# Optimization experiments

Measured on AMD Instinct MI355X. Metric: run time of the kernel, lower is better.

The kernel has to match this reference:

```python
import jax, jax.numpy as jnp
import numpy as np

NUM_LAYERS = 2


def setup_inputs() -> dict:
    key = jax.random.key(0)
    k1, k2, k3, k4 = jax.random.split(key, 4)
    N, E, D = 50000, 800000, 100
    features = jax.random.normal(k1, (N, D), dtype=jnp.float32)
    # stacked nn.Linear weights, one [D,D] per layer (no bias)
    W = jax.random.normal(k2, (NUM_LAYERS, D, D), dtype=jnp.float32) * 0.02
    src = jax.random.randint(k3, (E,), 0, N)
    dst = jax.random.randint(k4, (E,), 0, N)
    return {"features": features, "W": W, "src": src, "dst": dst}


def reference(features, W, src, dst):
    N, D = features.shape
    num_layers = W.shape[0]
    inv_lp1 = 1.0 / (num_layers + 1)

    # --- graph preprocessing (mirrors ItemConv.graph setter) ---
    # add self loops (fill_diag 1.0), then row-normalize by inverse degree
    loop = jnp.arange(N)
    src_all = jnp.concatenate([src, loop])  # message sources
    dst_all = jnp.concatenate([dst, loop])  # message destinations (rows of adj_t)
    deg = jax.ops.segment_sum(
        jnp.ones(src_all.shape, dtype=features.dtype), dst_all, num_segments=N
    )
    deg_inv = jnp.where(deg > 0, 1.0 / deg, 0.0)
    w = deg_inv[dst_all]  # per-edge weight: row-normalized, [E+N]

    # --- forward (LightGCN-style conv with linear projections) ---
    avg = features * inv_lp1
    x = features
    for i in range(num_layers):
        x = x @ W[i].T  # nn.Linear(D, D, bias=False)
        # SpMM: out[d] = sum_{e: dst=d} w_e * x[src_e]
        x = jax.ops.segment_sum(w[:, None] * x[src_all], dst_all, num_segments=N)
        # F.normalize(x): L2 along dim=-1 with eps=1e-12 (max-clamped norm)
        norm = jnp.linalg.norm(x, axis=-1, keepdims=True)
        avg = avg + (x / jnp.maximum(norm, 1e-12)) * inv_lp1
    return avg
```

## Files before the change

kernel.cpp:

```cpp
#include <hip/hip_runtime.h>

#define D 100
#define YSTRIDE 128
#define BSHIFT 7
#define BSIZE 128
#define BMASK 127
#define NBKMAX 512
#define EPB 2048
#define BCAP 4096
#define WTOT (2 * 7 * 4 * 64)

typedef __attribute__((ext_vector_type(8))) short bf8v;
typedef __attribute__((ext_vector_type(4))) float f4v;

__device__ inline unsigned short f2bf(float f) {
    unsigned u = __float_as_uint(f);
    return (unsigned short)((u + 0x7fffu + ((u >> 16) & 1u)) >> 16);
}
__device__ inline float bflo(unsigned v) { return __uint_as_float(v << 16); }
__device__ inline float bfhi(unsigned v) { return __uint_as_float(v & 0xffff0000u); }
__device__ inline unsigned short pk8(float a, float b) {
    return (unsigned short)(__builtin_amdgcn_cvt_pk_fp8_f32(a, b, 0, false) & 0xffff);
}

__device__ inline void acc8(float* acc, uint2 v, float w) {
    acc[0] = fmaf(__builtin_amdgcn_cvt_f32_fp8((int)v.x, 0), w, acc[0]);
    acc[1] = fmaf(__builtin_amdgcn_cvt_f32_fp8((int)v.x, 1), w, acc[1]);
    acc[2] = fmaf(__builtin_amdgcn_cvt_f32_fp8((int)v.x, 2), w, acc[2]);
    acc[3] = fmaf(__builtin_amdgcn_cvt_f32_fp8((int)v.x, 3), w, acc[3]);
    acc[4] = fmaf(__builtin_amdgcn_cvt_f32_fp8((int)v.y, 0), w, acc[4]);
    acc[5] = fmaf(__builtin_amdgcn_cvt_f32_fp8((int)v.y, 1), w, acc[5]);
    acc[6] = fmaf(__builtin_amdgcn_cvt_f32_fp8((int)v.y, 2), w, acc[6]);
    acc[7] = fmaf(__builtin_amdgcn_cvt_f32_fp8((int)v.y, 3), w, acc[7]);
}

__device__ inline void scan512_excl(int* a, int* t, int tid) {
    int v0 = a[2 * tid], v1 = a[2 * tid + 1];
    t[tid] = v0 + v1;
    __syncthreads();
    for (int off = 1; off < 256; off <<= 1) {
        int u = (tid >= off) ? t[tid - off] : 0;
        __syncthreads();
        t[tid] += u;
        __syncthreads();
    }
    int base = (tid ? t[tid - 1] : 0);
    a[2 * tid]     = base;
    a[2 * tid + 1] = base + v0;
    __syncthreads();
}

__global__ __launch_bounds__(256) void k_pre(const float* __restrict__ x0, const float* __restrict__ W,
                                             unsigned* __restrict__ s8, float* __restrict__ Wc,
                                             int* __restrict__ cur,
                                             int N, int packb) {
    int tid = threadIdx.x;
    int bx = blockIdx.x;

    if (bx < packb) {
        int t = bx * 256 + tid;
        if (t >= N * 32) return;
        int d = t >> 5, q = t & 31;
        unsigned p = 0u;
        if (q < D / 4) {
            float4 v = *(const float4*)(x0 + (long)d * D + q * 4);
            p = (unsigned)pk8(v.x, v.y) | ((unsigned)pk8(v.z, v.w) << 16);
        }
        s8[t] = p;
    } else if (bx == packb) {
        cur[tid] = 0;
        cur[tid + 256] = 0;
    } else {
        int t = (bx - packb - 1) * 256 + tid;
        if (t >= D * D) return;
        int i = t / D, j = t - i * D;
        const float* w2 = W + D * D + (long)i * D;
        float s = 0.f;
        for (int k = 0; k < D; k++) s += w2[k] * W[(long)k * D + j];
        Wc[t] = s;
    }
}

__global__ __launch_bounds__(256) void k_sortC(const int* __restrict__ src,
                                               const int* __restrict__ dst,
                                               int* __restrict__ cur,
                                               unsigned* __restrict__ ebuf, int E, int nbk,
                                               int nebk,
                                               const float* __restrict__ W1,
                                               const float* __restrict__ Wc,
                                               unsigned short* __restrict__ P) {
    __shared__ int lhist[NBKMAX], lstart[NBKMAX], runS[NBKMAX], t[256];
    __shared__ unsigned stage[EPB];
    int tid = threadIdx.x;

    if ((int)blockIdx.x >= nebk) {
        int t2 = ((int)blockIdx.x - nebk) * 256 + tid;
        if (t2 >= WTOT) return;
        int lane = t2 & 63;
        int r = t2 >> 6;
        int kt = r & 3;
        int r2 = r >> 2;
        int nt = r2 % 7;
        int l  = r2 / 7;
        const float* M = (l == 0) ? W1 : Wc;
        int ng = nt * 16 + (lane & 15);
        int k0 = kt * 32 + (lane >> 4) * 8;
        unsigned short u[8];
#pragma unroll
        for (int j = 0; j < 8; j++) {
            int k = k0 + j;
            u[j] = (ng < D && k < D) ? f2bf(M[(long)ng * D + k]) : (unsigned short)0;
        }
        uint4 o;
        o.x = (unsigned)u[0] | ((unsigned)u[1] << 16);
        o.y = (unsigned)u[2] | ((unsigned)u[3] << 16);
        o.z = (unsigned)u[4] | ((unsigned)u[5] << 16);
        o.w = (unsigned)u[6] | ((unsigned)u[7] << 16);
        *(uint4*)(P + (long)t2 * 8) = o;
        return;
    }

    int base = blockIdx.x * EPB;
    int count = min(EPB, E - base);

    for (int i = tid; i < NBKMAX; i += 256) lhist[i] = 0;
    __syncthreads();
    for (int i = tid; i < count; i += 256) atomicAdd(&lhist[dst[base + i] >> BSHIFT], 1);
    __syncthreads();
    for (int i = tid; i < NBKMAX; i += 256) lstart[i] = lhist[i];
    __syncthreads();
    scan512_excl(lstart, t, tid);
    for (int b = tid; b < nbk; b += 256) {
        int c = lhist[b];
        runS[b] = b * BCAP + (c ? atomicAdd(&cur[b], c) : 0);
    }
    __syncthreads();
    for (int i = tid; i < NBKMAX; i += 256) lhist[i] = 0;
    __syncthreads();
    for (int i = tid; i < count; i += 256) {
        int dv = dst[base + i];
        int sv = src[base + i];
        int b = dv >> BSHIFT;
        int r = atomicAdd(&lhist[b], 1);
        stage[lstart[b] + r] = ((unsigned)(dv & BMASK) << 16) | (unsigned)sv;
    }
    __syncthreads();
    int wave = tid >> 6, lane = tid & 63;
    for (int b = wave; b < nbk; b += 4) {
        int c = lhist[b], ls = lstart[b], rs = runS[b];
        for (int j = lane; j < c; j += 64) ebuf[rs + j] = stage[ls + j];
    }
}

__global__ __launch_bounds__(256) void k_csrD(const unsigned* __restrict__ ebuf,
                                              const int* __restrict__ cur,
                                              int* __restrict__ col,
                                              int* __restrict__ rps, int* __restrict__ rdeg,
                                              int N, int nbk) {
    __shared__ int lh[BSIZE], ls[BSIZE];
    __shared__ int colStage[BCAP];
    int b = blockIdx.x;
    int tid = threadIdx.x;
    int beg = b * BCAP;
    int cnt = cur[b];
    if (cnt > BCAP) cnt = BCAP;

    if (tid < BSIZE) lh[tid] = 0;
    __syncthreads();
    for (int i = tid; i < cnt; i += 256) atomicAdd(&lh[ebuf[beg + i] >> 16], 1);
    __syncthreads();
    if (tid < BSIZE) ls[tid] = lh[tid];
    __syncthreads();
    for (int off = 1; off < BSIZE; off <<= 1) {
        int v = (tid >= off && tid < BSIZE) ? ls[tid - off] : 0;
        __syncthreads();
        if (tid < BSIZE) ls[tid] += v;
        __syncthreads();
    }
    if (tid < BSIZE) ls[tid] -= lh[tid];
    __syncthreads();
    int d0 = b * BSIZE;
    if (tid < BSIZE && d0 + tid < N) {
        rps[d0 + tid]  = beg + ls[tid];
        rdeg[d0 + tid] = lh[tid];
    }
    if (tid < BSIZE) lh[tid] = 0;
    __syncthreads();
    for (int i = tid; i < cnt; i += 256) {
        unsigned p = ebuf[beg + i];
        int r = p >> 16, s = (int)(p & 0xffffu);
        int k = atomicAdd(&lh[r], 1);
        colStage[ls[r] + k] = s;
    }
    __syncthreads();
    for (int i = tid; i < cnt; i += 256) col[beg + i] = colStage[i];
}

__global__ __launch_bounds__(256) void k_spmm(const unsigned short* __restrict__ g8,
                                              const int* __restrict__ rps,
                                              const int* __restrict__ rdeg,
                                              const int* __restrict__ col,
                                              const unsigned* __restrict__ self16,
                                              unsigned short* __restrict__ o8,
                                              unsigned* __restrict__ o16,
                                              int write8, int N) {
    int wave = threadIdx.x >> 6;
    int lane = threadIdx.x & 63;
    int g = lane >> 4;
    int j = lane & 15;
    int d = blockIdx.x * 4 + wave;
    if (d >= N) return;

    int b0  = __builtin_amdgcn_readfirstlane(rps[d]);
    int deg = __builtin_amdgcn_readfirstlane(rdeg[d]);
    int e0 = b0 + deg;

    float acc[8];
    if (g == 0) {
        if (self16) {
            uint4 sv = *((const uint4*)(self16 + (long)d * 64) + j);
            acc[0] = bflo(sv.x); acc[1] = bfhi(sv.x);
            acc[2] = bflo(sv.y); acc[3] = bfhi(sv.y);
            acc[4] = bflo(sv.z); acc[5] = bfhi(sv.z);
            acc[6] = bflo(sv.w); acc[7] = bfhi(sv.w);
        } else {
            uint2 sv = *(const uint2*)(g8 + (long)d * 64 + j * 4);
#pragma unroll
            for (int k = 0; k < 8; k++) acc[k] = 0.f;
            acc8(acc, sv, 1.f);
        }
    } else {
#pragma unroll
        for (int k = 0; k < 8; k++) acc[k] = 0.f;
    }

    for (int win = b0; win < e0; win += 64) {
        int m = e0 - win;
        if (m > 64) m = 64;
        int c = col[win + lane];
        int t = 0;
        for (; t + 8 <= m; t += 8) {
            int sa = __shfl(c, t + g);
            int sb = __shfl(c, t + 4 + g);
            uint2 va = *(const uint2*)(g8 + (long)sa * 64 + j * 4);
            uint2 vb = *(const uint2*)(g8 + (long)sb * 64 + j * 4);
            acc8(acc, va, 1.f);
            acc8(acc, vb, 1.f);
        }
        for (; t < m; t += 4) {
            int rem = m - t;
            int idx = t + ((g < rem) ? g : 0);
            int sa = __shfl(c, idx);
            float w = (g < rem) ? 1.f : 0.f;
            uint2 va = *(const uint2*)(g8 + (long)sa * 64 + j * 4);
            acc8(acc, va, w);
        }
    }

#pragma unroll
    for (int k = 0; k < 8; k++) {
        acc[k] += __shfl_xor(acc[k], 16);
        acc[k] += __shfl_xor(acc[k], 32);
    }

    float dinv = 1.f / (float)(deg + 1);
    float r[8];
#pragma unroll
    for (int k = 0; k < 8; k++) r[k] = acc[k] * dinv;

    if (g == 0) {
        uint4 o;
        o.x = (unsigned)f2bf(r[0]) | ((unsigned)f2bf(r[1]) << 16);
        o.y = (unsigned)f2bf(r[2]) | ((unsigned)f2bf(r[3]) << 16);
        o.z = (unsigned)f2bf(r[4]) | ((unsigned)f2bf(r[5]) << 16);
        o.w = (unsigned)f2bf(r[6]) | ((unsigned)f2bf(r[7]) << 16);
        *((uint4*)(o16 + (long)d * 64) + j) = o;
    }
    if (write8 && g == 1) {
        uint2 p;
        p.x = (unsigned)pk8(r[0], r[1]) | ((unsigned)pk8(r[2], r[3]) << 16);
        p.y = (unsigned)pk8(r[4], r[5]) | ((unsigned)pk8(r[6], r[7]) << 16);
        *((uint2*)((unsigned*)o8 + (long)d * 32) + j) = p;
    }
}

__global__ __launch_bounds__(256) void k_epi(const unsigned short* __restrict__ u16,
                                             const unsigned short* __restrict__ v16,
                                             const unsigned short* __restrict__ P,
                                             const float* __restrict__ x0,
                                             float invlp1, float* __restrict__ out, int N) {
    int wave = threadIdx.x >> 6;
    int lane = threadIdx.x & 63;
    int quad = lane >> 4;
    int l16  = lane & 15;
    int rowbase = (blockIdx.x * 4 + wave) * 16;
    if (rowbase >= N) return;
    int arow = rowbase + l16;
    if (arow >= N) arow = N - 1;

    bf8v aU[4], aV[4];
    const unsigned short* ur = u16 + (long)arow * YSTRIDE;
    const unsigned short* vr = v16 + (long)arow * YSTRIDE;
#pragma unroll
    for (int kt = 0; kt < 4; kt++) {
        int k0 = kt * 32 + quad * 8;
        union { bf8v v; uint4 u; } a, b;
        a.u = *(const uint4*)(ur + k0);
        b.u = *(const uint4*)(vr + k0);
        aU[kt] = a.v;
        aV[kt] = b.v;
    }

    f4v accU[7], accV[7];
#pragma unroll
    for (int nt = 0; nt < 7; nt++) { accU[nt] = (f4v){0,0,0,0}; accV[nt] = (f4v){0,0,0,0}; }

    const uint4* bp = (const uint4*)P;
#pragma unroll
    for (int nt = 0; nt < 7; nt++) {
#pragma unroll
        for (int kt = 0; kt < 4; kt++) {
            union { uint4 u; bf8v v; } b1, b2;
            b1.u = bp[(nt * 4 + kt) * 64 + lane];
            b2.u = bp[(28 + nt * 4 + kt) * 64 + lane];
            accU[nt] = __builtin_amdgcn_mfma_f32_16x16x32_bf16(aU[kt], b1.v, accU[nt], 0, 0, 0);
            accV[nt] = __builtin_amdgcn_mfma_f32_16x16x32_bf16(aV[kt], b2.v, accV[nt], 0, 0, 0);
        }
    }

    float sU[4], sV[4];
#pragma unroll
    for (int i = 0; i < 4; i++) {
        float nu = 0.f, nv = 0.f;
#pragma unroll
        for (int nt = 0; nt < 7; nt++) {
            nu += accU[nt][i] * accU[nt][i];
            nv += accV[nt][i] * accV[nt][i];
        }
#pragma unroll
        for (int m = 1; m < 16; m <<= 1) {
            nu += __shfl_xor(nu, m);
            nv += __shfl_xor(nv, m);
        }
        sU[i] = invlp1 / fmaxf(sqrtf(nu), 1e-12f);
        sV[i] = invlp1 / fmaxf(sqrtf(nv), 1e-12f);
    }

#pragma unroll
    for (int nt = 0; nt < 7; nt++) {
        int cc = nt * 16 + l16;
        if (cc < D) {
#pragma unroll
            for (int i = 0; i < 4; i++) {
                int rr = rowbase + quad * 4 + i;
                if (rr < N) {
                    long idx = (long)rr * D + cc;
                    out[idx] = x0[idx] * invlp1 + accU[nt][i] * sU[i] + accV[nt][i] * sV[i];
                }
            }
        }
    }
}


extern "C" void kernel_launch(void* const* d_in, const int* in_sizes, int n_in,
                              void* d_out, int out_size, void* d_ws, size_t ws_size,
                              hipStream_t stream) {
    const float* features = (const float*)d_in[0];
    const float* W        = (const float*)d_in[1];
    const int*   src      = (const int*)d_in[2];
    const int*   dstv     = (const int*)d_in[3];

    int N = in_sizes[0] / D;
    int E = in_sizes[2];
    int L = in_sizes[1] / (D * D);
    float invlp1 = 1.f / (float)(L + 1);
    int NBK = (N + BSIZE - 1) >> BSHIFT;
    int nebk = (E + EPB - 1) / EPB;

    char*  ws  = (char*)d_ws;
    size_t off = 0;
    auto alloc = [&](size_t bytes) -> void* {
        void* p = (void*)(ws + off);
        off += (bytes + 255) & ~(size_t)255;
        return p;
    };
    unsigned*       s8     = (unsigned*)alloc((size_t)N * 32 * sizeof(unsigned));
    unsigned*       u8     = (unsigned*)alloc((size_t)N * 32 * sizeof(unsigned));
    unsigned*       u16    = (unsigned*)alloc((size_t)N * 64 * sizeof(unsigned));
    unsigned*       v16    = (unsigned*)alloc((size_t)N * 64 * sizeof(unsigned));
    float*          Wc     = (float*)alloc((size_t)D * D * sizeof(float));
    unsigned short* wpack  = (unsigned short*)alloc((size_t)WTOT * 8 * sizeof(unsigned short));
    unsigned*       ebuf   = (unsigned*)alloc((size_t)NBK * BCAP * sizeof(unsigned));
    int*            colb   = (int*)alloc((size_t)NBK * BCAP * sizeof(int));
    int*            rps    = (int*)alloc((size_t)N * sizeof(int));
    int*            rdeg   = (int*)alloc((size_t)N * sizeof(int));
    int*            cur    = (int*)alloc((size_t)NBKMAX * sizeof(int));

    int packb = (N * 32 + 255) / 256;
    int wcb   = (D * D + 255) / 256;
    int prepb = (WTOT + 255) / 256;

    k_pre<<<packb + 1 + wcb, 256, 0, stream>>>(features, W, s8, Wc, cur, N, packb);
    k_sortC<<<nebk + prepb, 256, 0, stream>>>(src, dstv, cur, ebuf, E, NBK, nebk, W, Wc, wpack);
    k_csrD<<<NBK, 256, 0, stream>>>(ebuf, cur, colb, rps, rdeg, N, NBK);

    int spmmblocks = (N + 3) / 4;
    k_spmm<<<spmmblocks, 256, 0, stream>>>((const unsigned short*)s8, rps, rdeg, colb,
                                           (const unsigned*)nullptr,
                                           (unsigned short*)u8, u16, 1, N);
    k_spmm<<<spmmblocks, 256, 0, stream>>>((const unsigned short*)u8, rps, rdeg, colb,
                                           u16, (unsigned short*)nullptr, v16, 0, N);

    int nrowtiles = (N + 15) / 16;
    int epiblocks = (nrowtiles + 3) / 4;
    k_epi<<<epiblocks, 256, 0, stream>>>((const unsigned short*)u16, (const unsigned short*)v16,
                                         wpack, features, invlp1, (float*)d_out, N);
}
```

Before: 198.1 us.

## Stage epilogue output in LDS for coalesced float4 stores; flatten bucket scatter

The epilogue kernel now writes the normalized projection results into a shared-memory tile and then streams the features read and the output write as contiguous float4 accesses per 64-row block. Before, each lane did scattered scalar loads and stores in MFMA layout. The sort kernel also encodes the bucket id in each staged edge word, so the copy to global memory is one flat loop over all edges instead of a per-bucket loop per wave. The later CSR kernel masks off the new bucket bits. This costs about 28KB of LDS per block and an extra barrier, which may reduce occupancy.

New measurement: 176.2 us, median of 2. 11.0% less time.

```diff
diff --git a/kernel.cpp b/kernel.cpp
--- a/kernel.cpp
+++ b/kernel.cpp
@@ -9,6 +9,7 @@
 #define EPB 2048
 #define BCAP 4096
 #define WTOT (2 * 7 * 4 * 64)
+#define OSTRIDE 112
 
 typedef __attribute__((ext_vector_type(8))) short bf8v;
 typedef __attribute__((ext_vector_type(4))) float f4v;
@@ -142,13 +143,13 @@
         int sv = src[base + i];
         int b = dv >> BSHIFT;
         int r = atomicAdd(&lhist[b], 1);
-        stage[lstart[b] + r] = ((unsigned)(dv & BMASK) << 16) | (unsigned)sv;
-    }
-    __syncthreads();
-    int wave = tid >> 6, lane = tid & 63;
-    for (int b = wave; b < nbk; b += 4) {
-        int c = lhist[b], ls = lstart[b], rs = runS[b];
-        for (int j = lane; j < c; j += 64) ebuf[rs + j] = stage[ls + j];
+        stage[lstart[b] + r] = ((unsigned)b << 23) | ((unsigned)(dv & BMASK) << 16) | (unsigned)sv;
+    }
+    __syncthreads();
+    for (int k = tid; k < count; k += 256) {
+        unsigned e = stage[k];
+        int b = (int)(e >> 23);
+        ebuf[runS[b] + (k - lstart[b])] = e;
     }
 }
 
@@ -167,7 +168,7 @@
 
     if (tid < BSIZE) lh[tid] = 0;
     __syncthreads();
-    for (int i = tid; i < cnt; i += 256) atomicAdd(&lh[ebuf[beg + i] >> 16], 1);
+    for (int i = tid; i < cnt; i += 256) atomicAdd(&lh[(ebuf[beg + i] >> 16) & BMASK], 1);
     __syncthreads();
     if (tid < BSIZE) ls[tid] = lh[tid];
     __syncthreads();
@@ -188,7 +189,7 @@
     __syncthreads();
     for (int i = tid; i < cnt; i += 256) {
         unsigned p = ebuf[beg + i];
-        int r = p >> 16, s = (int)(p & 0xffffu);
+        int r = (int)((p >> 16) & BMASK), s = (int)(p & 0xffffu);
         int k = atomicAdd(&lh[r], 1);
         colStage[ls[r] + k] = s;
     }
@@ -289,76 +290,97 @@
                                              const unsigned short* __restrict__ P,
                                              const float* __restrict__ x0,
                                              float invlp1, float* __restrict__ out, int N) {
-    int wave = threadIdx.x >> 6;
-    int lane = threadIdx.x & 63;
+    __shared__ float ot[64 * OSTRIDE];
+    int tid = threadIdx.x;
+    int wave = tid >> 6;
+    int lane = tid & 63;
     int quad = lane >> 4;
     int l16  = lane & 15;
-    int rowbase = (blockIdx.x * 4 + wave) * 16;
-    if (rowbase >= N) return;
-    int arow = rowbase + l16;
-    if (arow >= N) arow = N - 1;
-
-    bf8v aU[4], aV[4];
-    const unsigned short* ur = u16 + (long)arow * YSTRIDE;
-    const unsigned short* vr = v16 + (long)arow * YSTRIDE;
-#pragma unroll
-    for (int kt = 0; kt < 4; kt++) {
-        int k0 = kt * 32 + quad * 8;
-        union { bf8v v; uint4 u; } a, b;
-        a.u = *(const uint4*)(ur + k0);
-        b.u = *(const uint4*)(vr + k0);
-        aU[kt] = a.v;
-        aV[kt] = b.v;
-    }
-
-    f4v accU[7], accV[7];
-#pragma unroll
-    for (int nt = 0; nt < 7; nt++) { accU[nt] = (f4v){0,0,0,0}; accV[nt] = (f4v){0,0,0,0}; }
-
-    const uint4* bp = (const uint4*)P;
-#pragma unroll
-    for (int nt = 0; nt < 7; nt++) {
+    int blockbase = blockIdx.x * 64;
+    int rowbase = blockbase + wave * 16;
+
+    if (rowbase < N) {
+        int arow = rowbase + l16;
+        if (arow >= N) arow = N - 1;
+
+        bf8v aU[4], aV[4];
+        const unsigned short* ur = u16 + (long)arow * YSTRIDE;
+        const unsigned short* vr = v16 + (long)arow * YSTRIDE;
 #pragma unroll
         for (int kt = 0; kt < 4; kt++) {
-            union { uint4 u; bf8v v; } b1, b2;
-            b1.u = bp[(nt * 4 + kt) * 64 + lane];
-            b2.u = bp[(28 + nt * 4 + kt) * 64 + lane];
-            accU[nt] = __builtin_amdgcn_mfma_f32_16x16x32_bf16(aU[kt], b1.v, accU[nt], 0, 0, 0);
-            accV[nt] = __builtin_amdgcn_mfma_f32_16x16x32_bf16(aV[kt], b2.v, accV[nt], 0, 0, 0);
-        }
-    }
-
-    float sU[4], sV[4];
-#pragma unroll
-    for (int i = 0; i < 4; i++) {
-        float nu = 0.f, nv = 0.f;
+            int k0 = kt * 32 + quad * 8;
+            union { bf8v v; uint4 u; } a, b;
+            a.u = *(const uint4*)(ur + k0);
+            b.u = *(const uint4*)(vr + k0);
+            aU[kt] = a.v;
+            aV[kt] = b.v;
+        }
+
+        f4v accU[7], accV[7];
+#pragma unroll
+        for (int nt = 0; nt < 7; nt++) { accU[nt] = (f4v){0,0,0,0}; accV[nt] = (f4v){0,0,0,0}; }
+
+        const uint4* bp = (const uint4*)P;
 #pragma unroll
         for (int nt = 0; nt < 7; nt++) {
-            nu += accU[nt][i] * accU[nt][i];
-            nv += accV[nt][i] * accV[nt][i];
-        }
-#pragma unroll
-        for (int m = 1; m < 16; m <<= 1) {
-            nu += __shfl_xor(nu, m);
-            nv += __shfl_xor(nv, m);
-        }
-        sU[i] = invlp1 / fmaxf(sqrtf(nu), 1e-12f);
-        sV[i] = invlp1 / fmaxf(sqrtf(nv), 1e-12f);
-    }
-
-#pragma unroll
-    for (int nt = 0; nt < 7; nt++) {
-        int cc = nt * 16 + l16;
-        if (cc < D) {
-#pragma unroll
-            for (int i = 0; i < 4; i++) {
-                int rr = rowbase + quad * 4 + i;
-                if (rr < N) {
-                    long idx = (long)rr * D + cc;
-                    out[idx] = x0[idx] * invlp1 + accU[nt][i] * sU[i] + accV[nt][i] * sV[i];
+#pragma unroll
+            for (int kt = 0; kt < 4; kt++) {
+                union { uint4 u; bf8v v; } b1, b2;
+                b1.u = bp[(nt * 4 + kt) * 64 + lane];
+                b2.u = bp[(28 + nt * 4 + kt) * 64 + lane];
+                accU[nt] = __builtin_amdgcn_mfma_f32_16x16x32_bf16(aU[kt], b1.v, accU[nt], 0, 0, 0);
+                accV[nt] = __builtin_amdgcn_mfma_f32_16x16x32_bf16(aV[kt], b2.v, accV[nt], 0, 0, 0);
+            }
+        }
+
+        float sU[4], sV[4];
+#pragma unroll
+        for (int i = 0; i < 4; i++) {
+            float nu = 0.f, nv = 0.f;
+#pragma unroll
+            for (int nt = 0; nt < 7; nt++) {
+                nu += accU[nt][i] * accU[nt][i];
+                nv += accV[nt][i] * accV[nt][i];
+            }
+#pragma unroll
+            for (int m = 1; m < 16; m <<= 1) {
+                nu += __shfl_xor(nu, m);
+                nv += __shfl_xor(nv, m);
+            }
+            sU[i] = invlp1 / fmaxf(sqrtf(nu), 1e-12f);
+            sV[i] = invlp1 / fmaxf(sqrtf(nv), 1e-12f);
+        }
+
+#pragma unroll
+        for (int nt = 0; nt < 7; nt++) {
+            int cc = nt * 16 + l16;
+            if (cc < D) {
+#pragma unroll
+                for (int i = 0; i < 4; i++) {
+                    int lrow = wave * 16 + quad * 4 + i;
+                    ot[lrow * OSTRIDE + cc] = accU[nt][i] * sU[i] + accV[nt][i] * sV[i];
                 }
             }
         }
+    }
+    __syncthreads();
+
+    int nrows = N - blockbase;
+    if (nrows > 64) nrows = 64;
+    if (nrows <= 0) return;
+    int totalf = nrows * D;
+    long gbase = (long)blockbase * D;
+    for (int f = tid * 4; f < totalf; f += 256 * 4) {
+        int row = f / D;
+        int col = f - row * D;
+        float4 xv = *(const float4*)(x0 + gbase + f);
+        const float* lr = ot + row * OSTRIDE + col;
+        float4 ov;
+        ov.x = xv.x * invlp1 + lr[0];
+        ov.y = xv.y * invlp1 + lr[1];
+        ov.z = xv.z * invlp1 + lr[2];
+        ov.w = xv.w * invlp1 + lr[3];
+        *(float4*)(out + gbase + f) = ov;
     }
 }
 
@@ -412,8 +434,7 @@
     k_spmm<<<spmmblocks, 256, 0, stream>>>((const unsigned short*)u8, rps, rdeg, colb,
                                            u16, (unsigned short*)nullptr, v16, 0, N);
 
-    int nrowtiles = (N + 15) / 16;
-    int epiblocks = (nrowtiles + 3) / 4;
+    int epiblocks = (N + 63) / 64;
     k_epi<<<epiblocks, 256, 0, stream>>>((const unsigned short*)u16, (const unsigned short*)v16,
                                          wpack, features, invlp1, (float*)d_out, N);
 }
```
